# Kernel tuning notes

Measured on AMD Instinct MI355X. Metric: run time of the kernel, lower is better.

## Reference

```python
import jax, jax.numpy as jnp
import numpy as np

B, N, F, IMF = 16, 64, 512, 2048
EPS = 1e-5


def _linear_params(key, out_f, in_f):
    k1, k2 = jax.random.split(key)
    w = jax.random.normal(k1, (out_f, in_f), dtype=jnp.float32) * 0.02
    b = jax.random.normal(k2, (out_f,), dtype=jnp.float32) * 0.02
    return w, b


def setup_inputs() -> dict:
    key = jax.random.key(0)
    ks = jax.random.split(key, 8)
    inp = {}
    inp["input"] = jax.random.normal(ks[0], (B, N, F), dtype=jnp.float32)
    inp["im_input"] = jax.random.normal(ks[1], (B, IMF), dtype=jnp.float32)
    inp["gmlp1_w"], inp["gmlp1_b"] = _linear_params(ks[2], F, 2 * F)
    inp["gmlp2_w"], inp["gmlp2_b"] = _linear_params(ks[3], F, F)
    inp["gmlp3_w"], inp["gmlp3_b"] = _linear_params(ks[4], F, F)
    inp["im_w"], inp["im_b"] = _linear_params(ks[5], F, IMF)
    inp["bn_gamma"] = jnp.ones((F,), dtype=jnp.float32)
    inp["bn_beta"] = jnp.zeros((F,), dtype=jnp.float32)
    inp["d1_w"], inp["d1_b"] = _linear_params(ks[6], F, 2 * F)
    inp["d2_w"], inp["d2_b"] = _linear_params(ks[7], 2, F)
    return inp


def reference(input, im_input, gmlp1_w, gmlp1_b, gmlp2_w, gmlp2_b,
              gmlp3_w, gmlp3_b, im_w, im_b, bn_gamma, bn_beta,
              d1_w, d1_b, d2_w, d2_b):
    b, n, f = input.shape
    npair = n * n
    # relation_embedding: all-pairs expand + concat (replicating the exact
    # row-major reshape semantics of the original torch code, including the
    # memory-reinterpreting view used for feature2)
    feature1 = jnp.broadcast_to(input[:, None, :, :], (b, n, n, f)).reshape(b, npair, f)
    feature2 = jnp.broadcast_to(input[:, :, :, None], (b, n, f, n)).reshape(b, npair, f)
    feature = jnp.concatenate([feature1, feature2], axis=2).reshape(-1, 2 * f)  # [b*n^2, 1024]
    h = jax.nn.relu(feature @ gmlp1_w.T + gmlp1_b)
    h = jax.nn.relu(h @ gmlp2_w.T + gmlp2_b)
    h = jax.nn.relu(h @ gmlp3_w.T + gmlp3_b)
    sent_embedding = h.reshape(b, npair, f).mean(axis=1)  # [b, 512]
    # im_embedding: Linear + BatchNorm1d (training-mode batch stats) + ReLU
    img = im_input @ im_w.T + im_b
    mu = img.mean(axis=0)
    var = jnp.mean(jnp.square(img - mu), axis=0)  # biased variance
    img = bn_gamma * (img - mu) * jax.lax.rsqrt(var + EPS) + bn_beta
    img_embedding = jax.nn.relu(img)
    # net_D
    emb = jnp.concatenate([sent_embedding, img_embedding], axis=1)  # [b, 1024]
    out = jax.nn.relu(emb @ d1_w.T + d1_b) @ d2_w.T + d2_b  # [b, 2]
    return out
```

## Files before the change

### kernel.cpp

```cpp
#include <hip/hip_runtime.h>


typedef float f32x4 __attribute__((ext_vector_type(4)));
typedef __bf16 bf16x8v __attribute__((ext_vector_type(8)));
typedef long i64;

__device__ __forceinline__ unsigned cvt4_fp8(float a, float b, float c, float d) {
  unsigned v = 0;
  v = __builtin_amdgcn_cvt_pk_fp8_f32(a, b, v, false);
  v = __builtin_amdgcn_cvt_pk_fp8_f32(c, d, v, true);
  return v;
}

#define WS_A1Q     0u
#define WS_W1P     2097152u
#define WS_SENT    2129920u
#define WS_Y       2162688u
#define WS_IMGEMB  2195456u
#define WS_W2F8    2228224u
#define WS_W3F8    2490368u

__global__ __launch_bounds__(256) void k_conv(
    const float* __restrict__ input, const float* __restrict__ im_input,
    const float* __restrict__ g1w, const float* __restrict__ g1b,
    const float* __restrict__ g2w, const float* __restrict__ g3w,
    const float* __restrict__ imw, const float* __restrict__ imb,
    float* __restrict__ ws)
{
  __shared__ __align__(16) __bf16 xbuf[32768];
  const int blk = blockIdx.x, t = threadIdx.x;
  __bf16* w1p  = (__bf16*)((char*)ws + WS_W1P);
  float* sent  = (float*)((char*)ws + WS_SENT);
  float* yv    = (float*)((char*)ws + WS_Y);
  unsigned char* w2f8 = (unsigned char*)ws + WS_W2F8;
  unsigned char* w3f8 = (unsigned char*)ws + WS_W3F8;
  float* A1Qf = ws;

  if (blk < 256) {
    int idx = (blk * 256 + t) * 8;
    const float* src; unsigned char* dst; int off;
    if (idx < 262144) { src = g2w; dst = w2f8; off = idx; }
    else              { src = g3w; dst = w3f8; off = idx - 262144; }
    int o = off >> 9, k = off & 511;
    int ks = k >> 5, quad = (k >> 3) & 3;
    int doff = (o >> 4) * 8192 + ks * 512 + (quad * 16 + (o & 15)) * 8;
    float4 v0 = *(const float4*)(src + off);
    float4 v1 = *(const float4*)(src + off + 4);
    uint2 pk;
    pk.x = cvt4_fp8(v0.x, v0.y, v0.z, v0.w);
    pk.y = cvt4_fp8(v1.x, v1.y, v1.z, v1.w);
    *(uint2*)(dst + doff) = pk;
  } else if (blk < 272) {
    int idx = (blk - 256) * 256 + t;
    int o = idx >> 3, s = idx & 7;
    const float* p = g1w + (size_t)o * 1024 + 512 + s * 64;
    float sum = 0.f;
#pragma unroll
    for (int u = 0; u < 64; u += 4) {
      float4 v = *(const float4*)(p + u);
      sum += v.x + v.y + v.z + v.w;
    }
    int base = (o >> 4) * 512 + (o & 15) * 8 + s;
    w1p[base]       = (__bf16)sum;
    w1p[base + 128] = (__bf16)0.f;
    w1p[base + 256] = (__bf16)0.f;
    w1p[base + 384] = (__bf16)0.f;
    sent[idx] = 0.f; sent[idx + 4096] = 0.f;
  } else if (blk < 784) {
    int o = blk - 272;
    int wv = t >> 6, l = t & 63;
    const float* wrow = imw + (size_t)o * 2048;
    for (int bb = 0; bb < 4; ++bb) {
      int b = wv * 4 + bb;
      const float* xr = im_input + (size_t)b * 2048;
      float s = 0.f;
#pragma unroll
      for (int u = 0; u < 8; ++u) {
        int k = u * 256 + l * 4;
        float4 xv = *(const float4*)(xr + k);
        float4 wx = *(const float4*)(wrow + k);
        s += xv.x * wx.x + xv.y * wx.y + xv.z * wx.z + xv.w * wx.w;
      }
#pragma unroll
      for (int m = 32; m >= 1; m >>= 1) s += __shfl_xor(s, m);
      if (l == 0) yv[b * 512 + o] = s + imb[o];
    }
  } else {
    int pb = blk - 784;
    int b = pb >> 2, q = pb & 3;
#pragma unroll
    for (int it = 0; it < 16; ++it) {
      int id = t + 256 * it;
      int r = id >> 6, oc = id & 63;
      const float* src = input + (size_t)(b * 64 + r) * 512 + oc * 8;
      float4 v0 = *(const float4*)src;
      float4 v1 = *(const float4*)(src + 4);
      bf16x8v h;
      h[0] = (__bf16)v0.x; h[1] = (__bf16)v0.y; h[2] = (__bf16)v0.z; h[3] = (__bf16)v0.w;
      h[4] = (__bf16)v1.x; h[5] = (__bf16)v1.y; h[6] = (__bf16)v1.z; h[7] = (__bf16)v1.w;
      *(bf16x8v*)(xbuf + r * 512 + ((oc ^ (r & 7)) << 3)) = h;
    }
    __syncthreads();
    const int w = t >> 6, l = t & 63;
    const int quad = l >> 4, p16 = l & 15;
    const int msk3 = (p16 & 7) << 3;
    f32x4 acc2[2][4];
#pragma unroll
    for (int ot = 0; ot < 2; ++ot)
#pragma unroll
      for (int mt = 0; mt < 4; ++mt) { f32x4 z = {0.f, 0.f, 0.f, 0.f}; acc2[ot][mt] = z; }
    const float* wbase = g1w + (size_t)(q * 128 + w * 32 + p16) * 1024;
#pragma unroll 2
    for (int ks = 0; ks < 16; ++ks) {
      const int kcb = (((ks * 4 + quad) << 3) ^ msk3);
      bf16x8v bf[4];
#pragma unroll
      for (int mt = 0; mt < 4; ++mt)
        bf[mt] = *(const bf16x8v*)(xbuf + (p16 + 16 * mt) * 512 + kcb);
#pragma unroll
      for (int ot = 0; ot < 2; ++ot) {
        const float* ap = wbase + ot * 16384 + ks * 32 + quad * 8;
        float4 f0 = *(const float4*)ap;
        float4 f1 = *(const float4*)(ap + 4);
        bf16x8v af;
        af[0] = (__bf16)f0.x; af[1] = (__bf16)f0.y; af[2] = (__bf16)f0.z; af[3] = (__bf16)f0.w;
        af[4] = (__bf16)f1.x; af[5] = (__bf16)f1.y; af[6] = (__bf16)f1.z; af[7] = (__bf16)f1.w;
#pragma unroll
        for (int mt = 0; mt < 4; ++mt)
          acc2[ot][mt] = __builtin_amdgcn_mfma_f32_16x16x32_bf16(af, bf[mt], acc2[ot][mt], 0, 0, 0);
      }
    }
#pragma unroll
    for (int ot = 0; ot < 2; ++ot) {
      int o = q * 128 + w * 32 + ot * 16 + quad * 4;
      float4 bias = *(const float4*)(g1b + o);
      float bb[4] = {bias.x, bias.y, bias.z, bias.w};
      size_t o4 = (size_t)b * 128 + (o >> 2);
#pragma unroll
      for (int mt = 0; mt < 4; ++mt)
#pragma unroll
        for (int r = 0; r < 4; ++r)
          A1Qf[(o4 * 64 + mt * 16 + p16) * 4 + r] = acc2[ot][mt][r] + bb[r];
    }
  }
}

__device__ __forceinline__ void kloop8(const unsigned char* __restrict__ wl,
                                       const unsigned char* __restrict__ hbuf,
                                       int p16, int quad, f32x4 acc[4][8])
{
  const int msk3 = (p16 & 7) << 3;
  int moff[8];
#pragma unroll
  for (int mt = 0; mt < 8; ++mt)
    moff[mt] = (mt >> 2) * 32768 + (p16 + 16 * (mt & 3)) * 512;
  i64 a[4], an[4];
#pragma unroll
  for (int ot = 0; ot < 4; ++ot) a[ot] = *(const i64*)(wl + ot * 8192);
#pragma unroll 2
  for (int ks = 0; ks < 16; ++ks) {
    const int kcb = (((ks * 4 + quad) << 3) ^ msk3);
    i64 bf[8];
#pragma unroll
    for (int mt = 0; mt < 8; ++mt)
      bf[mt] = *(const i64*)(hbuf + moff[mt] + kcb);
    if (ks < 15) {
#pragma unroll
      for (int ot = 0; ot < 4; ++ot)
        an[ot] = *(const i64*)(wl + (ks + 1) * 512 + ot * 8192);
    }
#pragma unroll
    for (int ot = 0; ot < 4; ++ot)
#pragma unroll
      for (int mt = 0; mt < 4; ++mt)
        acc[ot][mt] = __builtin_amdgcn_mfma_f32_16x16x32_fp8_fp8(a[ot], bf[mt], acc[ot][mt], 0, 0, 0);
#pragma unroll
    for (int ot = 0; ot < 4; ++ot)
#pragma unroll
      for (int mt = 4; mt < 8; ++mt)
        acc[ot][mt] = __builtin_amdgcn_mfma_f32_16x16x32_fp8_fp8(a[ot], bf[mt], acc[ot][mt], 0, 0, 0);
    if (ks < 15) {
#pragma unroll
      for (int ot = 0; ot < 4; ++ot) a[ot] = an[ot];
    }
  }
}

__global__ __launch_bounds__(512, 2) void k_main(
    const float* __restrict__ input,
    const float* __restrict__ g2b, const float* __restrict__ g3b,
    const float* __restrict__ bng, const float* __restrict__ bnb,
    float* __restrict__ ws)
{
  const int blk = blockIdx.x, t = threadIdx.x;
  const float4* A1Q = (const float4*)ws;
  const __bf16* w1p = (const __bf16*)((char*)ws + WS_W1P);
  float* sent = (float*)((char*)ws + WS_SENT);
  float* yv   = (float*)((char*)ws + WS_Y);
  float* imge = (float*)((char*)ws + WS_IMGEMB);
  const unsigned char* w2f8 = (const unsigned char*)ws + WS_W2F8;
  const unsigned char* w3f8 = (const unsigned char*)ws + WS_W3F8;

  if (blk == 512) {
    int o = t;
    float vals[16];
    float mu = 0.f;
#pragma unroll
    for (int b = 0; b < 16; ++b) { vals[b] = yv[b * 512 + o]; mu += vals[b]; }
    mu *= (1.f / 16.f);
    float var = 0.f;
#pragma unroll
    for (int b = 0; b < 16; ++b) { float d = vals[b] - mu; var += d * d; }
    var *= (1.f / 16.f);
    float sc = bng[o] * rsqrtf(var + 1e-5f);
    float sh = bnb[o] - mu * sc;
#pragma unroll
    for (int b = 0; b < 16; ++b)
      imge[b * 512 + o] = fmaxf(vals[b] * sc + sh, 0.f);
    return;
  }

  __shared__ __align__(16) unsigned char hbuf8[65536];

  const int b = blk >> 5, ipair = blk & 31;
  const int w = t >> 6, l = t & 63;
  const int quad = l >> 4, p16 = l & 15;

  float xreg0[8], xreg1[8];
  {
    const float* xr0 = input + (size_t)(b * 64 + ipair * 2) * 512 + l * 8;
    *(float4*)xreg0       = *(const float4*)xr0;
    *(float4*)(xreg0 + 4) = *(const float4*)(xr0 + 4);
    *(float4*)xreg1       = *(const float4*)(xr0 + 512);
    *(float4*)(xreg1 + 4) = *(const float4*)(xr0 + 516);
  }

  f32x4 acc[4][8];

  {
    bf16x8v xb[8];
#pragma unroll
    for (int mt = 0; mt < 4; ++mt) {
#pragma unroll
      for (int j = 0; j < 8; ++j) {
        float v0 = __shfl(xreg0[j], p16 + 16 * mt);
        float v1 = __shfl(xreg1[j], p16 + 16 * mt);
        xb[mt][j]     = (quad == 0) ? (__bf16)v0 : (__bf16)0.f;
        xb[mt + 4][j] = (quad == 0) ? (__bf16)v1 : (__bf16)0.f;
      }
    }
#pragma unroll
    for (int ot = 0; ot < 4; ++ot)
#pragma unroll
      for (int mt = 0; mt < 8; ++mt) { f32x4 z = {0.f, 0.f, 0.f, 0.f}; acc[ot][mt] = z; }
#pragma unroll
    for (int ot = 0; ot < 4; ++ot) {
      bf16x8v af = *(const bf16x8v*)(w1p + (w * 4 + ot) * 512 + l * 8);
#pragma unroll
      for (int mt = 0; mt < 8; ++mt)
        acc[ot][mt] = __builtin_amdgcn_mfma_f32_16x16x32_bf16(af, xb[mt], acc[ot][mt], 0, 0, 0);
    }
    const float4* cq = A1Q + ((size_t)b * 128 + w * 16) * 64;
#pragma unroll
    for (int ot = 0; ot < 4; ++ot) {
#pragma unroll
      for (int mtp = 0; mtp < 4; ++mtp) {
        float4 c = cq[(ot * 4 + quad) * 64 + 16 * mtp + p16];
        int row = p16 + 16 * mtp;
        int col = w * 64 + ot * 16 + quad * 4;
        int addr = row * 512 + (((col >> 3) ^ (row & 7)) << 3) + (col & 7);
#pragma unroll
        for (int tau = 0; tau < 2; ++tau) {
          f32x4 v = acc[ot][tau * 4 + mtp];
          unsigned pk = cvt4_fp8(fmaxf(v[0] + c.x, 0.f), fmaxf(v[1] + c.y, 0.f),
                                 fmaxf(v[2] + c.z, 0.f), fmaxf(v[3] + c.w, 0.f));
          *(unsigned*)(hbuf8 + tau * 32768 + addr) = pk;
        }
      }
    }
  }
  __syncthreads();

#pragma unroll
  for (int ot = 0; ot < 4; ++ot)
#pragma unroll
    for (int mt = 0; mt < 8; ++mt) { f32x4 z = {0.f, 0.f, 0.f, 0.f}; acc[ot][mt] = z; }

  kloop8(w2f8 + (size_t)(w * 4) * 8192 + l * 8, hbuf8, p16, quad, acc);
  __syncthreads();
#pragma unroll
  for (int ot = 0; ot < 4; ++ot) {
    float4 b2 = *(const float4*)(g2b + w * 64 + ot * 16 + quad * 4);
#pragma unroll
    for (int mt = 0; mt < 8; ++mt) {
      f32x4 v = acc[ot][mt];
      unsigned pk = cvt4_fp8(fmaxf(v[0] + b2.x, 0.f), fmaxf(v[1] + b2.y, 0.f),
                             fmaxf(v[2] + b2.z, 0.f), fmaxf(v[3] + b2.w, 0.f));
      int row = p16 + 16 * (mt & 3);
      int col = w * 64 + ot * 16 + quad * 4;
      *(unsigned*)(hbuf8 + (mt >> 2) * 32768 + row * 512 +
                   (((col >> 3) ^ (row & 7)) << 3) + (col & 7)) = pk;
    }
  }
  __syncthreads();

#pragma unroll
  for (int ot = 0; ot < 4; ++ot)
#pragma unroll
    for (int mt = 0; mt < 8; ++mt) { f32x4 z = {0.f, 0.f, 0.f, 0.f}; acc[ot][mt] = z; }

  kloop8(w3f8 + (size_t)(w * 4) * 8192 + l * 8, hbuf8, p16, quad, acc);

#pragma unroll
  for (int ot = 0; ot < 4; ++ot) {
    float4 b3 = *(const float4*)(g3b + w * 64 + ot * 16 + quad * 4);
    float bb[4] = {b3.x, b3.y, b3.z, b3.w};
#pragma unroll
    for (int r = 0; r < 4; ++r) {
      float s = 0.f;
#pragma unroll
      for (int mt = 0; mt < 8; ++mt) s += fmaxf(acc[ot][mt][r] + bb[r], 0.f);
      s += __shfl_xor(s, 1);
      s += __shfl_xor(s, 2);
      s += __shfl_xor(s, 4);
      s += __shfl_xor(s, 8);
      if (p16 == 0)
        atomicAdd(&sent[b * 512 + w * 64 + ot * 16 + quad * 4 + r], s * (1.0f / 4096.0f));
    }
  }
}

__global__ __launch_bounds__(512) void k_head(
    const float* __restrict__ d1w, const float* __restrict__ d1b,
    const float* __restrict__ d2w, const float* __restrict__ d2b,
    const float* __restrict__ ws, float* __restrict__ out)
{
  __shared__ float emb[1024];
  __shared__ float red[8][2];
  const float* sent = (const float*)((const char*)ws + WS_SENT);
  const float* imge = (const float*)((const char*)ws + WS_IMGEMB);
  const int b = blockIdx.x, t = threadIdx.x;
  emb[t]       = sent[b * 512 + t];
  emb[512 + t] = imge[b * 512 + t];
  __syncthreads();
  const int v = t >> 6, l = t & 63;
  float p0 = 0.f, p1 = 0.f;
  for (int rr = 0; rr < 64; ++rr) {
    int row = v * 64 + rr;
    const float* wr = d1w + (size_t)row * 1024 + l * 4;
    float s = 0.f;
#pragma unroll
    for (int c = 0; c < 4; ++c) {
      float4 wv = *(const float4*)(wr + c * 256);
      float4 ev = *(const float4*)(emb + l * 4 + c * 256);
      s += wv.x * ev.x + wv.y * ev.y + wv.z * ev.z + wv.w * ev.w;
    }
#pragma unroll
    for (int m = 32; m >= 1; m >>= 1) s += __shfl_xor(s, m);
    float h = fmaxf(s + d1b[row], 0.f);
    p0 += d2w[row] * h;
    p1 += d2w[512 + row] * h;
  }
  if (l == 0) { red[v][0] = p0; red[v][1] = p1; }
  __syncthreads();
  if (t == 0) {
    float q0 = d2b[0], q1 = d2b[1];
#pragma unroll
    for (int u = 0; u < 8; ++u) { q0 += red[u][0]; q1 += red[u][1]; }
    out[b * 2 + 0] = q0;
    out[b * 2 + 1] = q1;
  }
}

extern "C" void kernel_launch(void* const* d_in, const int* in_sizes, int n_in,
                              void* d_out, int out_size, void* d_ws, size_t ws_size,
                              hipStream_t stream)
{
  const float* input    = (const float*)d_in[0];
  const float* im_input = (const float*)d_in[1];
  const float* g1w = (const float*)d_in[2];
  const float* g1b = (const float*)d_in[3];
  const float* g2w = (const float*)d_in[4];
  const float* g2b = (const float*)d_in[5];
  const float* g3w = (const float*)d_in[6];
  const float* g3b = (const float*)d_in[7];
  const float* imw = (const float*)d_in[8];
  const float* imb = (const float*)d_in[9];
  const float* bng = (const float*)d_in[10];
  const float* bnb = (const float*)d_in[11];
  const float* d1w = (const float*)d_in[12];
  const float* d1b = (const float*)d_in[13];
  const float* d2w = (const float*)d_in[14];
  const float* d2b = (const float*)d_in[15];
  float* out = (float*)d_out;
  float* ws  = (float*)d_ws;

  k_conv<<<848, 256, 0, stream>>>(input, im_input, g1w, g1b, g2w, g3w, imw, imb, ws);
  k_main<<<513, 512, 0, stream>>>(input, g2b, g3b, bng, bnb, ws);
  k_head<<<16, 512, 0, stream>>>(d1w, d1b, d2w, d2b, ws, out);
}
```

Baseline: 186.8 us.

## Switch FP8 GEMM inner loops to 16x16x128 scaled MFMA with repacked weights

Replaces the 16x16x32 FP8 MFMA K-loop for the second and third MLP layers with the gfx950 16x16x128 f8f6f4 scaled MFMA, using a unit scale (0x7F exponent). The FP8 weight repacking is changed so each lane reads 32 contiguous K bytes, and activation loads from LDS gather four 8-byte swizzled chunks per operand. This cuts the MFMA instruction count fourfold and shortens the K loop to 4 iterations, aiming to raise matrix-core throughput. The cost is wider register operands (i32x8 per tile plus double-buffered A), which may add register pressure at 512 threads and 2 blocks per CU.

```diff
diff --git a/kernel.cpp b/kernel.cpp
--- a/kernel.cpp
+++ b/kernel.cpp
@@ -3,6 +3,7 @@
 
 typedef float f32x4 __attribute__((ext_vector_type(4)));
 typedef __bf16 bf16x8v __attribute__((ext_vector_type(8)));
+typedef int i32x8 __attribute__((ext_vector_type(8)));
 typedef long i64;
 
 __device__ __forceinline__ unsigned cvt4_fp8(float a, float b, float c, float d) {
@@ -42,8 +43,7 @@
     if (idx < 262144) { src = g2w; dst = w2f8; off = idx; }
     else              { src = g3w; dst = w3f8; off = idx - 262144; }
     int o = off >> 9, k = off & 511;
-    int ks = k >> 5, quad = (k >> 3) & 3;
-    int doff = (o >> 4) * 8192 + ks * 512 + (quad * 16 + (o & 15)) * 8;
+    int doff = (o >> 4) * 8192 + (k >> 7) * 2048 + (((k >> 5) & 3) * 16 + (o & 15)) * 32 + (k & 31);
     float4 v0 = *(const float4*)(src + off);
     float4 v1 = *(const float4*)(src + off + 4);
     uint2 pk;
@@ -145,44 +145,65 @@
   }
 }
 
-__device__ __forceinline__ void kloop8(const unsigned char* __restrict__ wl,
-                                       const unsigned char* __restrict__ hbuf,
-                                       int p16, int quad, f32x4 acc[4][8])
+__device__ __forceinline__ void kloop128(const unsigned char* __restrict__ wl,
+                                         const unsigned char* __restrict__ hbuf,
+                                         int p16, int quad, f32x4 acc[4][8])
 {
-  const int msk3 = (p16 & 7) << 3;
+  const int msk = p16 & 7;
   int moff[8];
 #pragma unroll
   for (int mt = 0; mt < 8; ++mt)
     moff[mt] = (mt >> 2) * 32768 + (p16 + 16 * (mt & 3)) * 512;
-  i64 a[4], an[4];
-#pragma unroll
-  for (int ot = 0; ot < 4; ++ot) a[ot] = *(const i64*)(wl + ot * 8192);
-#pragma unroll 2
-  for (int ks = 0; ks < 16; ++ks) {
-    const int kcb = (((ks * 4 + quad) << 3) ^ msk3);
-    i64 bf[8];
-#pragma unroll
-    for (int mt = 0; mt < 8; ++mt)
-      bf[mt] = *(const i64*)(hbuf + moff[mt] + kcb);
-    if (ks < 15) {
-#pragma unroll
-      for (int ot = 0; ot < 4; ++ot)
-        an[ot] = *(const i64*)(wl + (ks + 1) * 512 + ot * 8192);
+  i32x8 a[2][4];
+#pragma unroll
+  for (int ot = 0; ot < 4; ++ot) {
+    union { i32x8 v; uint4 q[2]; } ua;
+    ua.q[0] = *(const uint4*)(wl + ot * 8192);
+    ua.q[1] = *(const uint4*)(wl + ot * 8192 + 16);
+    a[0][ot] = ua.v;
+  }
+#pragma unroll
+  for (int ks = 0; ks < 4; ++ks) {
+    const int cur = ks & 1, nxt = cur ^ 1;
+    const int cb = ks * 16 + quad * 4;
+    i32x8 bf[4];
+#pragma unroll
+    for (int mt = 0; mt < 4; ++mt) {
+      union { i32x8 v; i64 d[4]; } u;
+#pragma unroll
+      for (int dd = 0; dd < 4; ++dd)
+        u.d[dd] = *(const i64*)(hbuf + moff[mt] + (((cb + dd) ^ msk) << 3));
+      bf[mt] = u.v;
+    }
+    if (ks < 3) {
+#pragma unroll
+      for (int ot = 0; ot < 4; ++ot) {
+        union { i32x8 v; uint4 q[2]; } ua;
+        ua.q[0] = *(const uint4*)(wl + (ks + 1) * 2048 + ot * 8192);
+        ua.q[1] = *(const uint4*)(wl + (ks + 1) * 2048 + ot * 8192 + 16);
+        a[nxt][ot] = ua.v;
+      }
     }
 #pragma unroll
     for (int ot = 0; ot < 4; ++ot)
 #pragma unroll
       for (int mt = 0; mt < 4; ++mt)
-        acc[ot][mt] = __builtin_amdgcn_mfma_f32_16x16x32_fp8_fp8(a[ot], bf[mt], acc[ot][mt], 0, 0, 0);
+        acc[ot][mt] = __builtin_amdgcn_mfma_scale_f32_16x16x128_f8f6f4(
+            a[cur][ot], bf[mt], acc[ot][mt], 0, 0, 0, 0x7F7F7F7F, 0, 0x7F7F7F7F);
+#pragma unroll
+    for (int mt = 0; mt < 4; ++mt) {
+      union { i32x8 v; i64 d[4]; } u;
+#pragma unroll
+      for (int dd = 0; dd < 4; ++dd)
+        u.d[dd] = *(const i64*)(hbuf + moff[mt + 4] + (((cb + dd) ^ msk) << 3));
+      bf[mt] = u.v;
+    }
 #pragma unroll
     for (int ot = 0; ot < 4; ++ot)
 #pragma unroll
-      for (int mt = 4; mt < 8; ++mt)
-        acc[ot][mt] = __builtin_amdgcn_mfma_f32_16x16x32_fp8_fp8(a[ot], bf[mt], acc[ot][mt], 0, 0, 0);
-    if (ks < 15) {
-#pragma unroll
-      for (int ot = 0; ot < 4; ++ot) a[ot] = an[ot];
-    }
+      for (int mt = 0; mt < 4; ++mt)
+        acc[ot][mt + 4] = __builtin_amdgcn_mfma_scale_f32_16x16x128_f8f6f4(
+            a[cur][ot], bf[mt], acc[ot][mt + 4], 0, 0, 0, 0x7F7F7F7F, 0, 0x7F7F7F7F);
   }
 }
 
@@ -286,7 +307,7 @@
 #pragma unroll
     for (int mt = 0; mt < 8; ++mt) { f32x4 z = {0.f, 0.f, 0.f, 0.f}; acc[ot][mt] = z; }
 
-  kloop8(w2f8 + (size_t)(w * 4) * 8192 + l * 8, hbuf8, p16, quad, acc);
+  kloop128(w2f8 + (size_t)(w * 4) * 8192 + l * 32, hbuf8, p16, quad, acc);
   __syncthreads();
 #pragma unroll
   for (int ot = 0; ot < 4; ++ot) {
@@ -309,7 +330,7 @@
 #pragma unroll
     for (int mt = 0; mt < 8; ++mt) { f32x4 z = {0.f, 0.f, 0.f, 0.f}; acc[ot][mt] = z; }
 
-  kloop8(w3f8 + (size_t)(w * 4) * 8192 + l * 8, hbuf8, p16, quad, acc);
+  kloop128(w3f8 + (size_t)(w * 4) * 8192 + l * 32, hbuf8, p16, quad, acc);
 
 #pragma unroll
   for (int ot = 0; ot < 4; ++ot) {
```

Measured after the change: 266.5 us. 1.43x slower.
